# Performance work log

Hardware: AMD Instinct MI355X
Metric: run time of the kernel (lower is better)

## Reference

```python
import jax, jax.numpy as jnp
import numpy as np
import math

B, T, E, H, QL, SUB = 4, 2048, 64, 8, 6, 64  # batch, win_len, n_embd, n_head, q_len, sub_len


def _row_mask(index, sub_len, win_len):
    log_l = math.ceil(np.log2(sub_len))
    mask = np.zeros(win_len, dtype=np.float32)
    if (win_len // sub_len) * 2 * log_l > index:
        mask[: index + 1] = 1
    else:
        while index >= 0:
            if index - log_l + 1 < 0:
                mask[:index] = 1
                break
            mask[index - log_l + 1 : index + 1] = 1
            for i in range(log_l):
                new_index = index - log_l + 1 - 2 ** i
                if index - new_index <= sub_len and new_index >= 0:
                    mask[new_index] = 1
            index -= sub_len
    return mask


def _log_mask(win_len, sub_len):
    m = np.zeros((win_len, win_len), dtype=np.float32)
    for i in range(win_len):
        m[i] = _row_mask(i, sub_len, win_len)
    return m.reshape(1, 1, win_len, win_len)


def setup_inputs() -> dict:
    key = jax.random.key(0)
    ks = jax.random.split(key, 4)
    x = jax.random.normal(ks[0], (B, T, E), dtype=jnp.float32)
    Wqk = jax.random.normal(ks[1], (2 * H * E, E, QL), dtype=jnp.float32) * 0.02
    bqk = jnp.zeros((2 * H * E,), dtype=jnp.float32)
    Wv = jax.random.normal(ks[2], (E, H * E), dtype=jnp.float32) * 0.02
    bv = jnp.zeros((H * E,), dtype=jnp.float32)
    Wp = jax.random.normal(ks[3], (H * E, E), dtype=jnp.float32) * 0.02
    bp = jnp.zeros((E,), dtype=jnp.float32)
    mask = jnp.asarray(_log_mask(T, SUB).astype(bool))  # [1,1,T,T] bool
    return {"x": x, "Wqk": Wqk, "bqk": bqk, "Wv": Wv, "bv": bv,
            "Wp": Wp, "bp": bp, "mask": mask}


def reference(x, Wqk, bqk, Wv, bv, Wp, bp, mask):
    b, t, e = x.shape
    h = Wv.shape[1] // e
    ql = Wqk.shape[-1]

    # value projection (Conv1D rf=1 == dense)
    value = x @ Wv + bv                              # [B,T,H*E]

    # causal conv1d QK projection: left-pad by q_len-1
    xc = jnp.transpose(x, (0, 2, 1))                 # [B,E,T]
    qk = jax.lax.conv_general_dilated(
        xc, Wqk, window_strides=(1,), padding=[(ql - 1, 0)],
        dimension_numbers=("NCH", "OIH", "NCH"))    # [B,2*H*E,T]
    qk = qk + bqk[None, :, None]
    qk = jnp.transpose(qk, (0, 2, 1))                # [B,T,2*H*E]
    query, key_ = jnp.split(qk, 2, axis=2)

    q = query.reshape(b, t, h, e).transpose(0, 2, 1, 3)   # [B,H,T,E]
    k = key_.reshape(b, t, h, e).transpose(0, 2, 3, 1)    # [B,H,E,T]
    v = value.reshape(b, t, h, e).transpose(0, 2, 1, 3)   # [B,H,T,E]

    pre = jnp.einsum("bhqe,bhek->bhqk", q, k) / jnp.sqrt(jnp.asarray(e, x.dtype))
    m = mask[:, :, :t, :t].astype(pre.dtype)
    pre = pre * m + (-1e9) * (1.0 - m)
    attn_weights = jax.nn.softmax(pre, axis=-1)           # [B,H,T,T]
    # dropout p=0.0 -> identity
    attn = jnp.einsum("bhqk,bhke->bhqe", attn_weights, v)  # [B,H,T,E]
    attn = attn.transpose(0, 2, 1, 3).reshape(b, t, h * e)
    out = attn @ Wp + bp                                  # [B,T,E]
    return out, attn_weights
```

## Files before the change

kernel.cpp:

```cpp
#include <hip/hip_runtime.h>
#include <hip/hip_bf16.h>


typedef __attribute__((ext_vector_type(8))) short bf16x8;
typedef __attribute__((ext_vector_type(4))) float f32x4;

#define MFMA16(a, b, c) __builtin_amdgcn_mfma_f32_16x16x32_bf16((a), (b), (c), 0, 0, 0)

static __device__ __forceinline__ bool sparse_pred(int r, int c) {
  int d = r - c;
  if (d < 0) return false;
  int o = d & 63;
  int j = c + o;
  bool inS = (o <= 7) || (o == 9) || (o == 13) || (o == 21) || (o == 37);
  return (j >= 5) ? inS : (o >= 1);
}

__global__ void prep_kernel(const float* __restrict__ Wqk, const float* __restrict__ Wv,
                            __hip_bfloat16* __restrict__ Wt_qk, __hip_bfloat16* __restrict__ Wv_t) {
  int idx = blockIdx.x * 256 + threadIdx.x;
  if (idx < 1024 * 384) {
    int o = idx / 384, kidx = idx - o * 384;
    int kk = kidx >> 6, i = kidx & 63;
    Wt_qk[idx] = __float2bfloat16(Wqk[(o * 64 + i) * 6 + kk]);
  } else {
    int j = idx - 1024 * 384;
    int n = j >> 6, k = j & 63;
    Wv_t[j] = __float2bfloat16(Wv[k * 512 + n]);
  }
}

__global__ __launch_bounds__(256, 4) void proj_kernel(
    const float* __restrict__ x, const float* __restrict__ bqk, const float* __restrict__ bv,
    const __hip_bfloat16* __restrict__ Wt_qk, const __hip_bfloat16* __restrict__ Wv_t,
    __hip_bfloat16* __restrict__ q_bf, __hip_bfloat16* __restrict__ k_bf,
    __hip_bfloat16* __restrict__ v_bf) {
  const int tokTile = blockIdx.x;
  const int chTile = blockIdx.y;
  const int gt0 = tokTile * 64;
  const int b = gt0 >> 11;
  const int t0 = gt0 & 2047;
  const int thr = threadIdx.x;
  __shared__ __align__(16) __hip_bfloat16 xwin[69][72];
  __shared__ __align__(16) __hip_bfloat16 vt[64][72];

  for (int u = thr; u < 69 * 64; u += 256) {
    int row = u >> 6, i = u & 63;
    int t = t0 - 5 + row;
    float v = (t >= 0) ? x[((size_t)b * 2048 + t) * 64 + i] : 0.f;
    xwin[row][i] = __float2bfloat16(v);
  }
  __syncthreads();

  const int wave = thr >> 6, lane = thr & 63;
  const int lm = lane & 15, lq = lane >> 4;
  f32x4 acc[4];
#pragma unroll
  for (int nb = 0; nb < 4; ++nb) acc[nb] = (f32x4){0.f, 0.f, 0.f, 0.f};

  if (chTile < 16) {
    const int ch0 = chTile * 64;
    for (int kc = 0; kc < 12; ++kc) {
      int k0 = kc * 32 + lq * 8;
      int kk = k0 >> 6, i0 = k0 & 63;
      bf16x8 a = *reinterpret_cast<const bf16x8*>(&xwin[16 * wave + lm + kk][i0]);
#pragma unroll
      for (int nb = 0; nb < 4; ++nb) {
        bf16x8 bb =
            *reinterpret_cast<const bf16x8*>(&Wt_qk[(size_t)(ch0 + 16 * nb + lm) * 384 + k0]);
        acc[nb] = MFMA16(a, bb, acc[nb]);
      }
    }
#pragma unroll
    for (int nb = 0; nb < 4; ++nb) {
      int e = 16 * nb + lm;
      float bias = bqk[chTile * 64 + e];
#pragma unroll
      for (int reg = 0; reg < 4; ++reg)
        vt[16 * wave + lq * 4 + reg][e] = __float2bfloat16(acc[nb][reg] + bias);
    }
    __syncthreads();
    const int half = (chTile >> 3) & 1;
    const int h = chTile & 7;
    __hip_bfloat16* dst = half ? k_bf : q_bf;
    for (int u = thr; u < 512; u += 256) {
      int row = u >> 3, c8 = u & 7;
      *reinterpret_cast<uint4*>(dst + ((size_t)((b * 8 + h) * 2048 + t0 + row)) * 64 + c8 * 8) =
          *reinterpret_cast<const uint4*>(&vt[row][c8 * 8]);
    }
  } else {
    const int nv0 = (chTile - 16) * 64;
    for (int kc = 0; kc < 2; ++kc) {
      int i0 = kc * 32 + lq * 8;
      bf16x8 a = *reinterpret_cast<const bf16x8*>(&xwin[16 * wave + lm + 5][i0]);
#pragma unroll
      for (int nb = 0; nb < 4; ++nb) {
        bf16x8 bb = *reinterpret_cast<const bf16x8*>(&Wv_t[(size_t)(nv0 + 16 * nb + lm) * 64 + i0]);
        acc[nb] = MFMA16(a, bb, acc[nb]);
      }
    }
#pragma unroll
    for (int nb = 0; nb < 4; ++nb) {
      int e = 16 * nb + lm;
      float bias = bv[nv0 + e];
#pragma unroll
      for (int reg = 0; reg < 4; ++reg)
        vt[e][16 * wave + lq * 4 + reg] = __float2bfloat16(acc[nb][reg] + bias);
    }
    __syncthreads();
    const int h = chTile - 16;
    for (int u = thr; u < 512; u += 256) {
      int e = u >> 3, c8 = u & 7;
      *reinterpret_cast<uint4*>(v_bf + ((size_t)((b * 8 + h) * 64 + e)) * 2048 + t0 + c8 * 8) =
          *reinterpret_cast<const uint4*>(&vt[e][c8 * 8]);
    }
  }
}

__global__ __launch_bounds__(256, 2) void attn_kernel(
    const __hip_bfloat16* __restrict__ q_bf, const __hip_bfloat16* __restrict__ k_bf,
    const __hip_bfloat16* __restrict__ v_bf,
    float* __restrict__ attn, float* __restrict__ attnout) {
  const int bh = blockIdx.y;
  const int thr = threadIdx.x;
  const int wave = thr >> 6, lane = thr & 63;
  const int lm = lane & 15, lq = lane >> 4;

  __shared__ __align__(16) __hip_bfloat16 ps[4][16 * 72];
  __hip_bfloat16* psw = &ps[wave][0];

  const int b2 = bh >> 3, h = bh & 7;

  for (int task = 0; task < 2; ++task) {
    const int rt = (task == 0) ? (int)blockIdx.x : 31 - (int)blockIdx.x;
    const int r0 = rt * 64;
    const bool causal = (rt < 6);

    const __hip_bfloat16* qrow = q_bf + ((size_t)bh * 2048 + r0 + 16 * wave + lm) * 64;
    bf16x8 qa0 = *reinterpret_cast<const bf16x8*>(qrow + lq * 8);
    bf16x8 qa1 = *reinterpret_cast<const bf16x8*>(qrow + 32 + lq * 8);

    unsigned long long Mrow[4] = {~0ull, ~0ull, ~0ull, ~0ull};
    if (!causal) {
      const int S[12] = {0, 1, 2, 3, 4, 5, 6, 7, 9, 13, 21, 37};
#pragma unroll
      for (int reg = 0; reg < 4; ++reg) {
        int r64 = 16 * wave + 4 * lq + reg;
        unsigned long long m = 0;
#pragma unroll
        for (int i = 0; i < 12; ++i) m |= 1ull << ((r64 - S[i]) & 63);
        Mrow[reg] = m;
      }
    }

    float lsum[4] = {0.f, 0.f, 0.f, 0.f};
    for (int ct = 0; ct <= rt; ++ct) {
      const __hip_bfloat16* kbase = k_bf + ((size_t)bh * 2048 + ct * 64) * 64;
#pragma unroll
      for (int nb = 0; nb < 4; ++nb) {
        const __hip_bfloat16* krow = kbase + (size_t)(16 * nb + lm) * 64;
        bf16x8 kb0 = *reinterpret_cast<const bf16x8*>(krow + lq * 8);
        bf16x8 kb1 = *reinterpret_cast<const bf16x8*>(krow + 32 + lq * 8);
        f32x4 c = (f32x4){0.f, 0.f, 0.f, 0.f};
        c = MFMA16(qa0, kb0, c);
        c = MFMA16(qa1, kb1, c);
        const int col = ct * 64 + 16 * nb + lm;
        const int cbit = 16 * nb + lm;
#pragma unroll
        for (int reg = 0; reg < 4; ++reg) {
          const int row = r0 + 16 * wave + 4 * lq + reg;
          bool p;
          if (causal) {
            p = (col <= row);
          } else if (ct == 0) {
            p = sparse_pred(row, col);
          } else {
            p = (Mrow[reg] >> cbit) & 1ull;
            if (ct == rt) p = p && (col <= row);
          }
          float e = __expf(c[reg] * 0.125f);
          lsum[reg] += p ? e : 0.f;
        }
      }
    }
    float inv[4];
#pragma unroll
    for (int reg = 0; reg < 4; ++reg) {
      float v = lsum[reg];
      v += __shfl_xor(v, 1);
      v += __shfl_xor(v, 2);
      v += __shfl_xor(v, 4);
      v += __shfl_xor(v, 8);
      inv[reg] = 1.f / v;
    }

    f32x4 oacc[4];
#pragma unroll
    for (int eb = 0; eb < 4; ++eb) oacc[eb] = (f32x4){0.f, 0.f, 0.f, 0.f};

    for (int ct = 0; ct <= rt; ++ct) {
      const __hip_bfloat16* kbase = k_bf + ((size_t)bh * 2048 + ct * 64) * 64;
#pragma unroll
      for (int nb = 0; nb < 4; ++nb) {
        const __hip_bfloat16* krow = kbase + (size_t)(16 * nb + lm) * 64;
        bf16x8 kb0 = *reinterpret_cast<const bf16x8*>(krow + lq * 8);
        bf16x8 kb1 = *reinterpret_cast<const bf16x8*>(krow + 32 + lq * 8);
        f32x4 c = (f32x4){0.f, 0.f, 0.f, 0.f};
        c = MFMA16(qa0, kb0, c);
        c = MFMA16(qa1, kb1, c);
        const int col = ct * 64 + 16 * nb + lm;
        const int cbit = 16 * nb + lm;
#pragma unroll
        for (int reg = 0; reg < 4; ++reg) {
          const int row = r0 + 16 * wave + 4 * lq + reg;
          bool p;
          if (causal) {
            p = (col <= row);
          } else if (ct == 0) {
            p = sparse_pred(row, col);
          } else {
            p = (Mrow[reg] >> cbit) & 1ull;
            if (ct == rt) p = p && (col <= row);
          }
          float w = p ? __expf(c[reg] * 0.125f) * inv[reg] : 0.f;
          psw[(4 * lq + reg) * 72 + 16 * nb + lm] = __float2bfloat16(w);
          attn[((size_t)bh * 2048 + row) * 2048 + col] = w;
        }
      }
      bf16x8 pa0 = *reinterpret_cast<const bf16x8*>(psw + lm * 72 + lq * 8);
      bf16x8 pa1 = *reinterpret_cast<const bf16x8*>(psw + lm * 72 + 32 + lq * 8);
      const __hip_bfloat16* vbase = v_bf + ((size_t)bh * 64) * 2048 + ct * 64;
#pragma unroll
      for (int eb = 0; eb < 4; ++eb) {
        const __hip_bfloat16* vrow = vbase + (size_t)(16 * eb + lm) * 2048;
        bf16x8 vb0 = *reinterpret_cast<const bf16x8*>(vrow + lq * 8);
        bf16x8 vb1 = *reinterpret_cast<const bf16x8*>(vrow + 32 + lq * 8);
        oacc[eb] = MFMA16(pa0, vb0, oacc[eb]);
        oacc[eb] = MFMA16(pa1, vb1, oacc[eb]);
      }
    }

#pragma unroll
    for (int eb = 0; eb < 4; ++eb)
#pragma unroll
      for (int reg = 0; reg < 4; ++reg) {
        int row = r0 + 16 * wave + lq * 4 + reg;
        attnout[((size_t)(b2 * 2048 + row)) * 512 + h * 64 + 16 * eb + lm] = oacc[eb][reg];
      }
  }
}

__global__ __launch_bounds__(256, 4) void outproj_kernel(const float* __restrict__ attnout,
                                                         const float* __restrict__ Wp,
                                                         const float* __restrict__ bp,
                                                         float* __restrict__ out) {
  __shared__ __align__(16) float wp_s[128][64];
  const int thr = threadIdx.x;
  const int wave = thr >> 6, lane = thr & 63;
  const int row0 = blockIdx.x * 16 + wave * 4;
  float acc[4] = {0.f, 0.f, 0.f, 0.f};
  for (int kt = 0; kt < 4; ++kt) {
    __syncthreads();
    for (int u = thr; u < 2048; u += 256) {
      int r = u >> 4, c4 = (u & 15) * 4;
      *reinterpret_cast<float4*>(&wp_s[r][c4]) =
          *reinterpret_cast<const float4*>(&Wp[(size_t)(kt * 128 + r) * 64 + c4]);
    }
    __syncthreads();
    for (int k4 = 0; k4 < 32; ++k4) {
      float wv0 = wp_s[k4 * 4 + 0][lane];
      float wv1 = wp_s[k4 * 4 + 1][lane];
      float wv2 = wp_s[k4 * 4 + 2][lane];
      float wv3 = wp_s[k4 * 4 + 3][lane];
#pragma unroll
      for (int rr = 0; rr < 4; ++rr) {
        const float4 a = *reinterpret_cast<const float4*>(
            &attnout[(size_t)(row0 + rr) * 512 + kt * 128 + k4 * 4]);
        acc[rr] += a.x * wv0 + a.y * wv1 + a.z * wv2 + a.w * wv3;
      }
    }
  }
  const float bias = bp[lane];
#pragma unroll
  for (int rr = 0; rr < 4; ++rr) out[(size_t)(row0 + rr) * 64 + lane] = acc[rr] + bias;
}

extern "C" void kernel_launch(void* const* d_in, const int* in_sizes, int n_in, void* d_out,
                              int out_size, void* d_ws, size_t ws_size, hipStream_t stream) {
  (void)in_sizes;
  (void)n_in;
  (void)out_size;
  (void)ws_size;
  const float* x = (const float*)d_in[0];
  const float* Wqk = (const float*)d_in[1];
  const float* bqk = (const float*)d_in[2];
  const float* Wv = (const float*)d_in[3];
  const float* bv = (const float*)d_in[4];
  const float* Wp = (const float*)d_in[5];
  const float* bp = (const float*)d_in[6];

  float* out = (float*)d_out;
  float* attn = out + (size_t)4 * 2048 * 64;

  char* ws = (char*)d_ws;
  __hip_bfloat16* q_bf = (__hip_bfloat16*)(ws);
  __hip_bfloat16* k_bf = (__hip_bfloat16*)(ws + (size_t)8 * 1024 * 1024);
  __hip_bfloat16* v_bf = (__hip_bfloat16*)(ws + (size_t)16 * 1024 * 1024);
  float* attnout = (float*)(ws + (size_t)24 * 1024 * 1024);
  __hip_bfloat16* Wt_qk = (__hip_bfloat16*)(ws + (size_t)40 * 1024 * 1024);
  __hip_bfloat16* Wv_t = (__hip_bfloat16*)(ws + (size_t)41 * 1024 * 1024);

  hipLaunchKernelGGL(prep_kernel, dim3(1664), dim3(256), 0, stream, Wqk, Wv, Wt_qk, Wv_t);
  hipLaunchKernelGGL(proj_kernel, dim3(128, 24), dim3(256), 0, stream, x, bqk, bv, Wt_qk, Wv_t,
                     q_bf, k_bf, v_bf);
  hipLaunchKernelGGL(attn_kernel, dim3(16, 32), dim3(256), 0, stream, q_bf, k_bf, v_bf, attn,
                     attnout);
  hipLaunchKernelGGL(outproj_kernel, dim3(512), dim3(256), 0, stream, attnout, Wp, bp, out);
}
```

Measured before the change: 799.9 us.

## Split attention into row-sum pass and weighted-PV pass with chunked parallel sums

Replaces the single two-pass attention kernel with two kernels. The first computes softmax denominators over column chunks spread across more blocks, combining them with atomics into a zeroed buffer, and prefetches K fragments one tile ahead. The second kernel assigns one row tile per block, reads the precomputed sums, and writes the attention weights and P·V. This aims to improve load balance and occupancy across the triangular workload. The cost is an extra launch, a memset, and atomics on the sums buffer.

```diff
diff --git a/kernel.cpp b/kernel.cpp
--- a/kernel.cpp
+++ b/kernel.cpp
@@ -14,6 +14,23 @@
   int j = c + o;
   bool inS = (o <= 7) || (o == 9) || (o == 13) || (o == 21) || (o == 37);
   return (j >= 5) ? inS : (o >= 1);
+}
+
+struct KF {
+  bf16x8 a[8];
+};
+
+static __device__ __forceinline__ KF loadK(const __hip_bfloat16* __restrict__ kbh, int ct, int lm,
+                                           int lq) {
+  KF f;
+  const __hip_bfloat16* kbase = kbh + (size_t)ct * 64 * 64;
+#pragma unroll
+  for (int nb = 0; nb < 4; ++nb) {
+    const __hip_bfloat16* krow = kbase + (size_t)(16 * nb + lm) * 64;
+    f.a[2 * nb] = *reinterpret_cast<const bf16x8*>(krow + lq * 8);
+    f.a[2 * nb + 1] = *reinterpret_cast<const bf16x8*>(krow + 32 + lq * 8);
+  }
+  return f;
 }
 
 __global__ void prep_kernel(const float* __restrict__ Wqk, const float* __restrict__ Wv,
@@ -117,137 +134,224 @@
   }
 }
 
-__global__ __launch_bounds__(256, 2) void attn_kernel(
-    const __hip_bfloat16* __restrict__ q_bf, const __hip_bfloat16* __restrict__ k_bf,
-    const __hip_bfloat16* __restrict__ v_bf,
-    float* __restrict__ attn, float* __restrict__ attnout) {
-  const int bh = blockIdx.y;
+__global__ __launch_bounds__(256, 4) void attn_sums_kernel(const __hip_bfloat16* __restrict__ q_bf,
+                                                           const __hip_bfloat16* __restrict__ k_bf,
+                                                           float* __restrict__ sums) {
+  const int x = blockIdx.x, bh = blockIdx.y;
+  int rt, chunk;
+  if (x < 8) {
+    rt = x;
+    chunk = 0;
+  } else if (x < 24) {
+    rt = 8 + ((x - 8) >> 1);
+    chunk = (x - 8) & 1;
+  } else if (x < 48) {
+    rt = 16 + (x - 24) / 3;
+    chunk = (x - 24) % 3;
+  } else {
+    rt = 24 + ((x - 48) >> 2);
+    chunk = (x - 48) & 3;
+  }
+  const int ct0 = chunk * 8;
+  const int ct1 = min(ct0 + 8, rt + 1);
+  const int r0 = rt * 64;
+  const bool causal = (rt < 6);
+
   const int thr = threadIdx.x;
   const int wave = thr >> 6, lane = thr & 63;
   const int lm = lane & 15, lq = lane >> 4;
 
+  const __hip_bfloat16* qrow = q_bf + ((size_t)bh * 2048 + r0 + 16 * wave + lm) * 64;
+  bf16x8 qa0 = *reinterpret_cast<const bf16x8*>(qrow + lq * 8);
+  bf16x8 qa1 = *reinterpret_cast<const bf16x8*>(qrow + 32 + lq * 8);
+
+  unsigned pm[4] = {15u, 15u, 15u, 15u};
+  if (!causal) {
+    const int S[12] = {0, 1, 2, 3, 4, 5, 6, 7, 9, 13, 21, 37};
+#pragma unroll
+    for (int reg = 0; reg < 4; ++reg) {
+      int r64 = 16 * wave + 4 * lq + reg;
+      unsigned long long m = 0;
+#pragma unroll
+      for (int i = 0; i < 12; ++i) m |= 1ull << ((r64 - S[i]) & 63);
+      unsigned p = 0;
+#pragma unroll
+      for (int nb = 0; nb < 4; ++nb) p |= (unsigned)((m >> (16 * nb + lm)) & 1ull) << nb;
+      pm[reg] = p;
+    }
+  }
+
+  const __hip_bfloat16* kbh = k_bf + (size_t)bh * 2048 * 64;
+  float lsum[4] = {0.f, 0.f, 0.f, 0.f};
+  KF kc = loadK(kbh, ct0, lm, lq);
+  for (int ct = ct0; ct < ct1; ++ct) {
+    KF kn = kc;
+    if (ct + 1 < ct1) kn = loadK(kbh, ct + 1, lm, lq);
+    f32x4 cf[4];
+#pragma unroll
+    for (int nb = 0; nb < 4; ++nb) {
+      f32x4 c = (f32x4){0.f, 0.f, 0.f, 0.f};
+      c = MFMA16(qa0, kc.a[2 * nb], c);
+      c = MFMA16(qa1, kc.a[2 * nb + 1], c);
+      cf[nb] = c;
+    }
+    const bool diag = (ct == rt);
+    if (causal ? !diag : false) {
+#pragma unroll
+      for (int nb = 0; nb < 4; ++nb)
+#pragma unroll
+        for (int reg = 0; reg < 4; ++reg) lsum[reg] += __expf(cf[nb][reg] * 0.125f);
+    } else if (causal) {
+#pragma unroll
+      for (int nb = 0; nb < 4; ++nb) {
+        const int col = ct * 64 + 16 * nb + lm;
+#pragma unroll
+        for (int reg = 0; reg < 4; ++reg) {
+          const int row = r0 + 16 * wave + 4 * lq + reg;
+          lsum[reg] += (col <= row) ? __expf(cf[nb][reg] * 0.125f) : 0.f;
+        }
+      }
+    } else if (ct == 0) {
+#pragma unroll
+      for (int nb = 0; nb < 4; ++nb) {
+        const int col = 16 * nb + lm;
+#pragma unroll
+        for (int reg = 0; reg < 4; ++reg) {
+          const int row = r0 + 16 * wave + 4 * lq + reg;
+          lsum[reg] += sparse_pred(row, col) ? __expf(cf[nb][reg] * 0.125f) : 0.f;
+        }
+      }
+    } else if (!diag) {
+#pragma unroll
+      for (int nb = 0; nb < 4; ++nb)
+#pragma unroll
+        for (int reg = 0; reg < 4; ++reg)
+          lsum[reg] += ((pm[reg] >> nb) & 1u) ? __expf(cf[nb][reg] * 0.125f) : 0.f;
+    } else {
+#pragma unroll
+      for (int nb = 0; nb < 4; ++nb) {
+        const int col = ct * 64 + 16 * nb + lm;
+#pragma unroll
+        for (int reg = 0; reg < 4; ++reg) {
+          const int row = r0 + 16 * wave + 4 * lq + reg;
+          bool p = ((pm[reg] >> nb) & 1u) && (col <= row);
+          lsum[reg] += p ? __expf(cf[nb][reg] * 0.125f) : 0.f;
+        }
+      }
+    }
+    kc = kn;
+  }
+#pragma unroll
+  for (int reg = 0; reg < 4; ++reg) {
+    float v = lsum[reg];
+    v += __shfl_xor(v, 1);
+    v += __shfl_xor(v, 2);
+    v += __shfl_xor(v, 4);
+    v += __shfl_xor(v, 8);
+    if (lm == reg) atomicAdd(&sums[(size_t)bh * 2048 + r0 + 16 * wave + 4 * lq + reg], v);
+  }
+}
+
+__global__ __launch_bounds__(256, 4) void attn_pv_kernel(
+    const __hip_bfloat16* __restrict__ q_bf, const __hip_bfloat16* __restrict__ k_bf,
+    const __hip_bfloat16* __restrict__ v_bf,
+    const float* __restrict__ sums, float* __restrict__ attn, float* __restrict__ attnout) {
+  const int rt = 31 - (int)blockIdx.x;
+  const int bh = blockIdx.y;
+  const int r0 = rt * 64;
+  const bool causal = (rt < 6);
+  const int thr = threadIdx.x;
+  const int wave = thr >> 6, lane = thr & 63;
+  const int lm = lane & 15, lq = lane >> 4;
+
   __shared__ __align__(16) __hip_bfloat16 ps[4][16 * 72];
   __hip_bfloat16* psw = &ps[wave][0];
 
+  const __hip_bfloat16* qrow = q_bf + ((size_t)bh * 2048 + r0 + 16 * wave + lm) * 64;
+  bf16x8 qa0 = *reinterpret_cast<const bf16x8*>(qrow + lq * 8);
+  bf16x8 qa1 = *reinterpret_cast<const bf16x8*>(qrow + 32 + lq * 8);
+
+  float inv[4];
+#pragma unroll
+  for (int reg = 0; reg < 4; ++reg)
+    inv[reg] = 1.f / sums[(size_t)bh * 2048 + r0 + 16 * wave + 4 * lq + reg];
+
+  unsigned pm[4] = {15u, 15u, 15u, 15u};
+  if (!causal) {
+    const int S[12] = {0, 1, 2, 3, 4, 5, 6, 7, 9, 13, 21, 37};
+#pragma unroll
+    for (int reg = 0; reg < 4; ++reg) {
+      int r64 = 16 * wave + 4 * lq + reg;
+      unsigned long long m = 0;
+#pragma unroll
+      for (int i = 0; i < 12; ++i) m |= 1ull << ((r64 - S[i]) & 63);
+      unsigned p = 0;
+#pragma unroll
+      for (int nb = 0; nb < 4; ++nb) p |= (unsigned)((m >> (16 * nb + lm)) & 1ull) << nb;
+      pm[reg] = p;
+    }
+  }
+
+  f32x4 oacc[4];
+#pragma unroll
+  for (int eb = 0; eb < 4; ++eb) oacc[eb] = (f32x4){0.f, 0.f, 0.f, 0.f};
+
+  const __hip_bfloat16* kbh = k_bf + (size_t)bh * 2048 * 64;
+  const __hip_bfloat16* vbh = v_bf + (size_t)bh * 64 * 2048;
+  float* arow0 = attn + ((size_t)bh * 2048 + r0 + 16 * wave + 4 * lq) * 2048;
+
+  for (int ct = 0; ct <= rt; ++ct) {
+    KF kc = loadK(kbh, ct, lm, lq);
+    f32x4 cf[4];
+#pragma unroll
+    for (int nb = 0; nb < 4; ++nb) {
+      f32x4 c = (f32x4){0.f, 0.f, 0.f, 0.f};
+      c = MFMA16(qa0, kc.a[2 * nb], c);
+      c = MFMA16(qa1, kc.a[2 * nb + 1], c);
+      cf[nb] = c;
+    }
+    const bool diag = (ct == rt);
+#pragma unroll
+    for (int nb = 0; nb < 4; ++nb) {
+      const int col = ct * 64 + 16 * nb + lm;
+#pragma unroll
+      for (int reg = 0; reg < 4; ++reg) {
+        const int row = r0 + 16 * wave + 4 * lq + reg;
+        bool p;
+        if (causal) {
+          p = diag ? (col <= row) : true;
+        } else if (ct == 0) {
+          p = sparse_pred(row, col);
+        } else {
+          p = (pm[reg] >> nb) & 1u;
+          if (diag) p = p && (col <= row);
+        }
+        float w = p ? __expf(cf[nb][reg] * 0.125f) * inv[reg] : 0.f;
+        psw[(4 * lq + reg) * 72 + 16 * nb + lm] = __float2bfloat16(w);
+        arow0[(size_t)reg * 2048 + col] = w;
+      }
+    }
+    bf16x8 pa0 = *reinterpret_cast<const bf16x8*>(psw + lm * 72 + lq * 8);
+    bf16x8 pa1 = *reinterpret_cast<const bf16x8*>(psw + lm * 72 + 32 + lq * 8);
+    const __hip_bfloat16* vbase = vbh + ct * 64;
+#pragma unroll
+    for (int eb = 0; eb < 4; ++eb) {
+      const __hip_bfloat16* vrow = vbase + (size_t)(16 * eb + lm) * 2048;
+      bf16x8 vb0 = *reinterpret_cast<const bf16x8*>(vrow + lq * 8);
+      bf16x8 vb1 = *reinterpret_cast<const bf16x8*>(vrow + 32 + lq * 8);
+      oacc[eb] = MFMA16(pa0, vb0, oacc[eb]);
+      oacc[eb] = MFMA16(pa1, vb1, oacc[eb]);
+    }
+  }
+
   const int b2 = bh >> 3, h = bh & 7;
-
-  for (int task = 0; task < 2; ++task) {
-    const int rt = (task == 0) ? (int)blockIdx.x : 31 - (int)blockIdx.x;
-    const int r0 = rt * 64;
-    const bool causal = (rt < 6);
-
-    const __hip_bfloat16* qrow = q_bf + ((size_t)bh * 2048 + r0 + 16 * wave + lm) * 64;
-    bf16x8 qa0 = *reinterpret_cast<const bf16x8*>(qrow + lq * 8);
-    bf16x8 qa1 = *reinterpret_cast<const bf16x8*>(qrow + 32 + lq * 8);
-
-    unsigned long long Mrow[4] = {~0ull, ~0ull, ~0ull, ~0ull};
-    if (!causal) {
-      const int S[12] = {0, 1, 2, 3, 4, 5, 6, 7, 9, 13, 21, 37};
-#pragma unroll
-      for (int reg = 0; reg < 4; ++reg) {
-        int r64 = 16 * wave + 4 * lq + reg;
-        unsigned long long m = 0;
-#pragma unroll
-        for (int i = 0; i < 12; ++i) m |= 1ull << ((r64 - S[i]) & 63);
-        Mrow[reg] = m;
-      }
-    }
-
-    float lsum[4] = {0.f, 0.f, 0.f, 0.f};
-    for (int ct = 0; ct <= rt; ++ct) {
-      const __hip_bfloat16* kbase = k_bf + ((size_t)bh * 2048 + ct * 64) * 64;
-#pragma unroll
-      for (int nb = 0; nb < 4; ++nb) {
-        const __hip_bfloat16* krow = kbase + (size_t)(16 * nb + lm) * 64;
-        bf16x8 kb0 = *reinterpret_cast<const bf16x8*>(krow + lq * 8);
-        bf16x8 kb1 = *reinterpret_cast<const bf16x8*>(krow + 32 + lq * 8);
-        f32x4 c = (f32x4){0.f, 0.f, 0.f, 0.f};
-        c = MFMA16(qa0, kb0, c);
-        c = MFMA16(qa1, kb1, c);
-        const int col = ct * 64 + 16 * nb + lm;
-        const int cbit = 16 * nb + lm;
-#pragma unroll
-        for (int reg = 0; reg < 4; ++reg) {
-          const int row = r0 + 16 * wave + 4 * lq + reg;
-          bool p;
-          if (causal) {
-            p = (col <= row);
-          } else if (ct == 0) {
-            p = sparse_pred(row, col);
-          } else {
-            p = (Mrow[reg] >> cbit) & 1ull;
-            if (ct == rt) p = p && (col <= row);
-          }
-          float e = __expf(c[reg] * 0.125f);
-          lsum[reg] += p ? e : 0.f;
-        }
-      }
-    }
-    float inv[4];
+#pragma unroll
+  for (int eb = 0; eb < 4; ++eb)
 #pragma unroll
     for (int reg = 0; reg < 4; ++reg) {
-      float v = lsum[reg];
-      v += __shfl_xor(v, 1);
-      v += __shfl_xor(v, 2);
-      v += __shfl_xor(v, 4);
-      v += __shfl_xor(v, 8);
-      inv[reg] = 1.f / v;
-    }
-
-    f32x4 oacc[4];
-#pragma unroll
-    for (int eb = 0; eb < 4; ++eb) oacc[eb] = (f32x4){0.f, 0.f, 0.f, 0.f};
-
-    for (int ct = 0; ct <= rt; ++ct) {
-      const __hip_bfloat16* kbase = k_bf + ((size_t)bh * 2048 + ct * 64) * 64;
-#pragma unroll
-      for (int nb = 0; nb < 4; ++nb) {
-        const __hip_bfloat16* krow = kbase + (size_t)(16 * nb + lm) * 64;
-        bf16x8 kb0 = *reinterpret_cast<const bf16x8*>(krow + lq * 8);
-        bf16x8 kb1 = *reinterpret_cast<const bf16x8*>(krow + 32 + lq * 8);
-        f32x4 c = (f32x4){0.f, 0.f, 0.f, 0.f};
-        c = MFMA16(qa0, kb0, c);
-        c = MFMA16(qa1, kb1, c);
-        const int col = ct * 64 + 16 * nb + lm;
-        const int cbit = 16 * nb + lm;
-#pragma unroll
-        for (int reg = 0; reg < 4; ++reg) {
-          const int row = r0 + 16 * wave + 4 * lq + reg;
-          bool p;
-          if (causal) {
-            p = (col <= row);
-          } else if (ct == 0) {
-            p = sparse_pred(row, col);
-          } else {
-            p = (Mrow[reg] >> cbit) & 1ull;
-            if (ct == rt) p = p && (col <= row);
-          }
-          float w = p ? __expf(c[reg] * 0.125f) * inv[reg] : 0.f;
-          psw[(4 * lq + reg) * 72 + 16 * nb + lm] = __float2bfloat16(w);
-          attn[((size_t)bh * 2048 + row) * 2048 + col] = w;
-        }
-      }
-      bf16x8 pa0 = *reinterpret_cast<const bf16x8*>(psw + lm * 72 + lq * 8);
-      bf16x8 pa1 = *reinterpret_cast<const bf16x8*>(psw + lm * 72 + 32 + lq * 8);
-      const __hip_bfloat16* vbase = v_bf + ((size_t)bh * 64) * 2048 + ct * 64;
-#pragma unroll
-      for (int eb = 0; eb < 4; ++eb) {
-        const __hip_bfloat16* vrow = vbase + (size_t)(16 * eb + lm) * 2048;
-        bf16x8 vb0 = *reinterpret_cast<const bf16x8*>(vrow + lq * 8);
-        bf16x8 vb1 = *reinterpret_cast<const bf16x8*>(vrow + 32 + lq * 8);
-        oacc[eb] = MFMA16(pa0, vb0, oacc[eb]);
-        oacc[eb] = MFMA16(pa1, vb1, oacc[eb]);
-      }
-    }
-
-#pragma unroll
-    for (int eb = 0; eb < 4; ++eb)
-#pragma unroll
-      for (int reg = 0; reg < 4; ++reg) {
-        int row = r0 + 16 * wave + lq * 4 + reg;
-        attnout[((size_t)(b2 * 2048 + row)) * 512 + h * 64 + 16 * eb + lm] = oacc[eb][reg];
-      }
-  }
+      int row = r0 + 16 * wave + lq * 4 + reg;
+      attnout[((size_t)(b2 * 2048 + row)) * 512 + h * 64 + 16 * eb + lm] = oacc[eb][reg];
+    }
 }
 
 __global__ __launch_bounds__(256, 4) void outproj_kernel(const float* __restrict__ attnout,
@@ -309,11 +413,14 @@
   float* attnout = (float*)(ws + (size_t)24 * 1024 * 1024);
   __hip_bfloat16* Wt_qk = (__hip_bfloat16*)(ws + (size_t)40 * 1024 * 1024);
   __hip_bfloat16* Wv_t = (__hip_bfloat16*)(ws + (size_t)41 * 1024 * 1024);
-
+  float* sums = (float*)(ws + (size_t)42 * 1024 * 1024);
+
+  hipMemsetAsync(sums, 0, (size_t)32 * 2048 * sizeof(float), stream);
   hipLaunchKernelGGL(prep_kernel, dim3(1664), dim3(256), 0, stream, Wqk, Wv, Wt_qk, Wv_t);
   hipLaunchKernelGGL(proj_kernel, dim3(128, 24), dim3(256), 0, stream, x, bqk, bv, Wt_qk, Wv_t,
                      q_bf, k_bf, v_bf);
-  hipLaunchKernelGGL(attn_kernel, dim3(16, 32), dim3(256), 0, stream, q_bf, k_bf, v_bf, attn,
-                     attnout);
+  hipLaunchKernelGGL(attn_sums_kernel, dim3(80, 32), dim3(256), 0, stream, q_bf, k_bf, sums);
+  hipLaunchKernelGGL(attn_pv_kernel, dim3(32, 32), dim3(256), 0, stream, q_bf, k_bf, v_bf, sums,
+                     attn, attnout);
   hipLaunchKernelGGL(outproj_kernel, dim3(512), dim3(256), 0, stream, attnout, Wp, bp, out);
 }
```

Result: slower. 904.7 us (+13.1%).
